# Kernel optimization log

Hardware: AMD Instinct MI355X
Metric: run time of the kernel (lower is better)

## Reference

```python
import jax, jax.numpy as jnp
import numpy as np

# Hyperparameters (from __init__ defaults)
TIME_RES = 25
BASE_RES = 512
MAX_RES = 32768
N_LEVELS = 8
N_FEATS = 4
LOG2_HASHMAP = 13
HASHMAP_SIZE = 1 << LOG2_HASHMAP  # 8192
PRIME_Y = np.uint32(2654435761)   # instant-ngp 2D hash prime (dim0 prime is 1)

# Per-level grid scales (tcnn convention: scale = 2^(l*log2_pls)*base - 1)
_LOG2_PLS = np.log2(MAX_RES / BASE_RES) / (N_LEVELS - 1)
SCALES = jnp.asarray(np.exp2(np.arange(N_LEVELS) * _LOG2_PLS) * BASE_RES - 1.0,
                     dtype=jnp.float32)  # [L]


def _hash_encode(x, table_t):
    """Instant-NGP 2D multires hash encoding for one time slice.
    x: [N,2] in [0,1); table_t: [L, H, F]. Returns [N, L*F].
    All levels satisfy res^2 > HASHMAP_SIZE, so always the hash path."""
    N = x.shape[0]
    pos = x[:, None, :] * SCALES[None, :, None] + 0.5        # [N,L,2]
    pos_i = jnp.floor(pos)
    frac = pos - pos_i                                        # [N,L,2]
    pos_i = pos_i.astype(jnp.uint32)
    lvl = jnp.arange(N_LEVELS, dtype=jnp.int32)[None, :]      # [1,L]
    acc = jnp.zeros((N, N_LEVELS, N_FEATS), dtype=table_t.dtype)
    mask = jnp.uint32(HASHMAP_SIZE - 1)
    for dx in (0, 1):  # 4 bilinear corners (static unroll)
        for dy in (0, 1):
            ix = pos_i[..., 0] + jnp.uint32(dx)               # [N,L]
            iy = pos_i[..., 1] + jnp.uint32(dy)
            h = jnp.bitwise_xor(ix, iy * PRIME_Y) & mask      # [N,L] hash index
            w = (frac[..., 0] if dx else 1.0 - frac[..., 0]) * \
                (frac[..., 1] if dy else 1.0 - frac[..., 1])  # [N,L]
            f = table_t[lvl, h.astype(jnp.int32)]             # [N,L,F] gather
            acc = acc + w[..., None] * f
    return acc.reshape(N, N_LEVELS * N_FEATS)


def setup_inputs() -> dict:
    key = jax.random.key(0)
    k1, k2 = jax.random.split(key)
    N = 2_000_000
    x = jax.random.uniform(k1, (N, 2), dtype=jnp.float32)
    t = jnp.asarray(0.3, dtype=jnp.float32)  # scalar time in [0,1]
    # tcnn initializes hash tables uniform in [-1e-4, 1e-4]
    table = jax.random.uniform(k2, (TIME_RES, N_LEVELS, HASHMAP_SIZE, N_FEATS),
                               dtype=jnp.float32, minval=-1e-4, maxval=1e-4)
    return {"x": x, "t": t, "table": table}


def reference(x, t, table):
    idx = t * (TIME_RES - 1)
    i1 = jnp.floor(idx).astype(jnp.int32)
    i2 = jnp.ceil(idx).astype(jnp.int32)
    # blend weight; equals (i2-idx, idx-i1) when i1!=i2 and (1,0) when equal,
    # matching the torch branch semantics.
    w2 = idx - i1.astype(idx.dtype)
    w1 = 1.0 - w2
    tab1 = jax.lax.dynamic_index_in_dim(table, i1, axis=0, keepdims=False)
    tab2 = jax.lax.dynamic_index_in_dim(table, i2, axis=0, keepdims=False)
    f1 = _hash_encode(x, tab1)  # [N, 32]
    f2 = _hash_encode(x, tab2)
    return w1 * f1 + w2 * f2
```

## Files before the change

### kernel.cpp

```cpp
#include <hip/hip_runtime.h>
#include <hip/hip_fp16.h>
#include <math.h>

#define NLV 8
#define NF 4
#define HSZ 8192
#define TRES 25
#define PRIME 2654435761u

struct Scales { float s[NLV]; };

__global__ __launch_bounds__(256) void blend_kernel(
    const float* __restrict__ table, const float* __restrict__ tptr,
    __half2* __restrict__ bt)
{
    int i = blockIdx.x * 256 + threadIdx.x;
    float t = *tptr;
    float idx = t * (float)(TRES - 1);
    float fi1 = floorf(idx);
    float fi2 = ceilf(idx);
    float w2 = idx - fi1;
    float w1 = 1.0f - w2;
    size_t off1 = (size_t)(int)fi1 * (size_t)(NLV * HSZ * NF);
    size_t off2 = (size_t)(int)fi2 * (size_t)(NLV * HSZ * NF);
    float4 a = ((const float4*)(table + off1))[i];
    float4 b = ((const float4*)(table + off2))[i];
    float4 r;
    r.x = w1 * a.x + w2 * b.x;
    r.y = w1 * a.y + w2 * b.y;
    r.z = w1 * a.z + w2 * b.z;
    r.w = w1 * a.w + w2 * b.w;
    bt[2 * (size_t)i]     = __floats2half2_rn(r.x, r.y);
    bt[2 * (size_t)i + 1] = __floats2half2_rn(r.z, r.w);
}

__device__ __forceinline__ float2 h2f(unsigned u) {
    return __half22float2(__builtin_bit_cast(__half2, u));
}

__device__ __forceinline__ float4 gather_lvl(const uint2* tbl, float2 p, float scale)
{
    float px = __fadd_rn(__fmul_rn(p.x, scale), 0.5f);
    float py = __fadd_rn(__fmul_rn(p.y, scale), 0.5f);
    float fx0 = floorf(px), fy0 = floorf(py);
    float fx = px - fx0, fy = py - fy0;
    unsigned ix = (unsigned)(int)fx0;
    unsigned iy = (unsigned)(int)fy0;
    unsigned hy0 = iy * PRIME;
    unsigned hy1 = hy0 + PRIME;
    unsigned h00 = (ix         ^ hy0) & (HSZ - 1);
    unsigned h01 = (ix         ^ hy1) & (HSZ - 1);
    unsigned h10 = ((ix + 1u)  ^ hy0) & (HSZ - 1);
    unsigned h11 = ((ix + 1u)  ^ hy1) & (HSZ - 1);
    uint2 v00 = tbl[h00];
    uint2 v01 = tbl[h01];
    uint2 v10 = tbl[h10];
    uint2 v11 = tbl[h11];
    float gx = 1.0f - fx, gy = 1.0f - fy;
    float w00 = gx * gy, w01 = gx * fy, w10 = fx * gy, w11 = fx * fy;
    float2 a00 = h2f(v00.x), b00 = h2f(v00.y);
    float2 a01 = h2f(v01.x), b01 = h2f(v01.y);
    float2 a10 = h2f(v10.x), b10 = h2f(v10.y);
    float2 a11 = h2f(v11.x), b11 = h2f(v11.y);
    float4 r;
    r.x = w00 * a00.x + w01 * a01.x + w10 * a10.x + w11 * a11.x;
    r.y = w00 * a00.y + w01 * a01.y + w10 * a10.y + w11 * a11.y;
    r.z = w00 * b00.x + w01 * b01.x + w10 * b10.x + w11 * b11.x;
    r.w = w00 * b00.y + w01 * b01.y + w10 * b10.y + w11 * b11.y;
    return r;
}

__global__ __launch_bounds__(1024, 4) void encode_kernel(
    const float* __restrict__ x, const float4* __restrict__ bt,
    float* __restrict__ out, int npts, Scales sc)
{
    __shared__ float4 smem[2][4096];
    int tid = threadIdx.x;
    int base = blockIdx.x * 4096 + tid;
    int n0 = base, n1 = base + 1024, n2 = base + 2048, n3 = base + 3072;
    int c0 = n0 < npts ? n0 : npts - 1;
    int c1 = n1 < npts ? n1 : npts - 1;
    int c2 = n2 < npts ? n2 : npts - 1;
    int c3 = n3 < npts ? n3 : npts - 1;
    float2 p0 = ((const float2*)x)[c0];
    float2 p1 = ((const float2*)x)[c1];
    float2 p2 = ((const float2*)x)[c2];
    float2 p3 = ((const float2*)x)[c3];

    float4 acc[4][4];

    {
        const float4* src = bt;
        float4 s0 = src[tid], s1 = src[tid + 1024],
               s2 = src[tid + 2048], s3 = src[tid + 3072];
        smem[0][tid] = s0; smem[0][tid + 1024] = s1;
        smem[0][tid + 2048] = s2; smem[0][tid + 3072] = s3;
    }
    __syncthreads();

    #pragma unroll
    for (int l = 0; l < NLV; ++l) {
        float4 s0, s1, s2, s3;
        if (l < NLV - 1) {
            const float4* src = bt + (size_t)(l + 1) * 4096;
            s0 = src[tid];        s1 = src[tid + 1024];
            s2 = src[tid + 2048]; s3 = src[tid + 3072];
        }

        const uint2* tbl = (const uint2*)smem[l & 1];
        float scale = sc.s[l];
        acc[0][l & 3] = gather_lvl(tbl, p0, scale);
        acc[1][l & 3] = gather_lvl(tbl, p1, scale);
        acc[2][l & 3] = gather_lvl(tbl, p2, scale);
        acc[3][l & 3] = gather_lvl(tbl, p3, scale);

        if (l < NLV - 1) {
            float4* dst = smem[(l & 1) ^ 1];
            dst[tid] = s0; dst[tid + 1024] = s1;
            dst[tid + 2048] = s2; dst[tid + 3072] = s3;
        }

        if ((l & 3) == 3) {
            int g = l >> 2;
            if (n0 < npts) {
                float4* o = (float4*)(out + (size_t)n0 * 32) + g * 4;
                o[0] = acc[0][0]; o[1] = acc[0][1]; o[2] = acc[0][2]; o[3] = acc[0][3];
            }
            if (n1 < npts) {
                float4* o = (float4*)(out + (size_t)n1 * 32) + g * 4;
                o[0] = acc[1][0]; o[1] = acc[1][1]; o[2] = acc[1][2]; o[3] = acc[1][3];
            }
            if (n2 < npts) {
                float4* o = (float4*)(out + (size_t)n2 * 32) + g * 4;
                o[0] = acc[2][0]; o[1] = acc[2][1]; o[2] = acc[2][2]; o[3] = acc[2][3];
            }
            if (n3 < npts) {
                float4* o = (float4*)(out + (size_t)n3 * 32) + g * 4;
                o[0] = acc[3][0]; o[1] = acc[3][1]; o[2] = acc[3][2]; o[3] = acc[3][3];
            }
        }
        __syncthreads();
    }
}

extern "C" void kernel_launch(void* const* d_in, const int* in_sizes, int n_in,
                              void* d_out, int out_size, void* d_ws, size_t ws_size,
                              hipStream_t stream) {
    const float* x     = (const float*)d_in[0];
    const float* t     = (const float*)d_in[1];
    const float* table = (const float*)d_in[2];
    float* out = (float*)d_out;
    __half2* bt = (__half2*)d_ws;

    int npts = in_sizes[0] / 2;

    Scales sc;
    const double l2p = log2(32768.0 / 512.0) / 7.0;
    for (int l = 0; l < NLV; ++l)
        sc.s[l] = (float)(exp2((double)l * l2p) * 512.0 - 1.0);

    blend_kernel<<<(NLV * HSZ) / 256, 256, 0, stream>>>(table, t, bt);

    int nblocks = (npts + 4095) / 4096;
    encode_kernel<<<nblocks, 1024, 0, stream>>>(
        x, (const float4*)bt, out, npts, sc);
}
```

Baseline: 460.7 us.

## Halve points per block and write each point's full feature row at the end

Each block now handles 2048 points (two per thread) instead of 4096, so the grid doubles to 977 blocks. Each thread holds all 8 levels' results in registers and writes its 32 output floats in one contiguous burst, replacing the two partial writes per group of four levels. The final-level barrier is also dropped. The trade-off is that the per-block shared-memory table load (the full 128KB blended table) is now spread over half as many points, doubling total table staging traffic.

New measurement: 459.6 us. Within noise of the previous version (-0.2%).

```diff
diff --git a/kernel.cpp b/kernel.cpp
--- a/kernel.cpp
+++ b/kernel.cpp
@@ -76,25 +76,21 @@
 {
     __shared__ float4 smem[2][4096];
     int tid = threadIdx.x;
-    int base = blockIdx.x * 4096 + tid;
-    int n0 = base, n1 = base + 1024, n2 = base + 2048, n3 = base + 3072;
+    int base = blockIdx.x * 2048 + tid;
+    int n0 = base, n1 = base + 1024;
     int c0 = n0 < npts ? n0 : npts - 1;
     int c1 = n1 < npts ? n1 : npts - 1;
-    int c2 = n2 < npts ? n2 : npts - 1;
-    int c3 = n3 < npts ? n3 : npts - 1;
     float2 p0 = ((const float2*)x)[c0];
     float2 p1 = ((const float2*)x)[c1];
-    float2 p2 = ((const float2*)x)[c2];
-    float2 p3 = ((const float2*)x)[c3];
 
-    float4 acc[4][4];
+    float4 acc0[NLV], acc1[NLV];
 
     {
         const float4* src = bt;
-        float4 s0 = src[tid], s1 = src[tid + 1024],
-               s2 = src[tid + 2048], s3 = src[tid + 3072];
-        smem[0][tid] = s0; smem[0][tid + 1024] = s1;
-        smem[0][tid + 2048] = s2; smem[0][tid + 3072] = s3;
+        smem[0][tid]        = src[tid];
+        smem[0][tid + 1024] = src[tid + 1024];
+        smem[0][tid + 2048] = src[tid + 2048];
+        smem[0][tid + 3072] = src[tid + 3072];
     }
     __syncthreads();
 
@@ -109,37 +105,26 @@
 
         const uint2* tbl = (const uint2*)smem[l & 1];
         float scale = sc.s[l];
-        acc[0][l & 3] = gather_lvl(tbl, p0, scale);
-        acc[1][l & 3] = gather_lvl(tbl, p1, scale);
-        acc[2][l & 3] = gather_lvl(tbl, p2, scale);
-        acc[3][l & 3] = gather_lvl(tbl, p3, scale);
+        acc0[l] = gather_lvl(tbl, p0, scale);
+        acc1[l] = gather_lvl(tbl, p1, scale);
 
         if (l < NLV - 1) {
             float4* dst = smem[(l & 1) ^ 1];
             dst[tid] = s0; dst[tid + 1024] = s1;
             dst[tid + 2048] = s2; dst[tid + 3072] = s3;
+            __syncthreads();
         }
+    }
 
-        if ((l & 3) == 3) {
-            int g = l >> 2;
-            if (n0 < npts) {
-                float4* o = (float4*)(out + (size_t)n0 * 32) + g * 4;
-                o[0] = acc[0][0]; o[1] = acc[0][1]; o[2] = acc[0][2]; o[3] = acc[0][3];
-            }
-            if (n1 < npts) {
-                float4* o = (float4*)(out + (size_t)n1 * 32) + g * 4;
-                o[0] = acc[1][0]; o[1] = acc[1][1]; o[2] = acc[1][2]; o[3] = acc[1][3];
-            }
-            if (n2 < npts) {
-                float4* o = (float4*)(out + (size_t)n2 * 32) + g * 4;
-                o[0] = acc[2][0]; o[1] = acc[2][1]; o[2] = acc[2][2]; o[3] = acc[2][3];
-            }
-            if (n3 < npts) {
-                float4* o = (float4*)(out + (size_t)n3 * 32) + g * 4;
-                o[0] = acc[3][0]; o[1] = acc[3][1]; o[2] = acc[3][2]; o[3] = acc[3][3];
-            }
-        }
-        __syncthreads();
+    if (n0 < npts) {
+        float4* o = (float4*)(out + (size_t)n0 * 32);
+        #pragma unroll
+        for (int l = 0; l < NLV; ++l) o[l] = acc0[l];
+    }
+    if (n1 < npts) {
+        float4* o = (float4*)(out + (size_t)n1 * 32);
+        #pragma unroll
+        for (int l = 0; l < NLV; ++l) o[l] = acc1[l];
     }
 }
 
@@ -161,7 +146,7 @@
 
     blend_kernel<<<(NLV * HSZ) / 256, 256, 0, stream>>>(table, t, bt);
 
-    int nblocks = (npts + 4095) / 4096;
+    int nblocks = (npts + 2047) / 2048;
     encode_kernel<<<nblocks, 1024, 0, stream>>>(
         x, (const float4*)bt, out, npts, sc);
 }
```
